# Kernel optimization log

Hardware: AMD Instinct MI355X
Metric: run time of the kernel (lower is better)

## Reference

```python
import jax, jax.numpy as jnp
import numpy as np

T, B = 64, 32
POS_V, WORD_V = 48, 32000
P_EMB, W_EMB = 128, 512
P_HID, W_HID = 256, 1024


def setup_inputs() -> dict:
    key = jax.random.key(0)
    ks = iter(jax.random.split(key, 40))
    def prm(shape, s=0.05):
        return jax.random.normal(next(ks), shape, dtype=jnp.float32) * s
    z = lambda *shape: jnp.zeros(shape, jnp.float32)
    inp = {
        'pos': jax.random.randint(next(ks), (T, B), 0, POS_V),
        'word': jax.random.randint(next(ks), (T, B), 0, WORD_V),
        'pos_emb_W': prm((POS_V, P_EMB)),
        'word_emb_W': prm((WORD_V, W_EMB)),
        'w2p_W': prm((W_HID, W_HID)), 'w2p_b': z(W_HID),
        'p2w_W': prm((P_HID, P_HID)), 'p2w_b': z(P_HID),
        'p_Wih0': prm((4 * P_HID, P_EMB + W_HID)), 'p_Whh0': prm((4 * P_HID, P_HID)),
        'p_bih0': z(4 * P_HID), 'p_bhh0': z(4 * P_HID),
        'w_Wih0': prm((4 * W_HID, W_EMB + P_HID)), 'w_Whh0': prm((4 * W_HID, W_HID)),
        'w_bih0': z(4 * W_HID), 'w_bhh0': z(4 * W_HID),
        'w_Wih1': prm((4 * W_HID, W_HID)), 'w_Whh1': prm((4 * W_HID, W_HID)),
        'w_bih1': z(4 * W_HID), 'w_bhh1': z(4 * W_HID),
        'pos_proj_W': prm((POS_V, P_HID)), 'pos_proj_b': z(POS_V),
        'word_proj1_W': prm((W_EMB, W_HID)), 'word_proj1_b': z(W_EMB),
        'word_proj2_b': z(WORD_V),
    }
    return inp


def _lstm_cell(x, h, c, Wih, Whh, bih, bhh):
    # PyTorch LSTMCell: gates ordered i, f, g, o
    g = x @ Wih.T + h @ Whh.T + bih + bhh
    i, f, gg, o = jnp.split(g, 4, axis=-1)
    c_new = jax.nn.sigmoid(f) * c + jax.nn.sigmoid(i) * jnp.tanh(gg)
    h_new = jax.nn.sigmoid(o) * jnp.tanh(c_new)
    return h_new, c_new


def reference(pos, word, pos_emb_W, word_emb_W, w2p_W, w2p_b, p2w_W, p2w_b,
              p_Wih0, p_Whh0, p_bih0, p_bhh0,
              w_Wih0, w_Whh0, w_bih0, w_bhh0,
              w_Wih1, w_Whh1, w_bih1, w_bhh1,
              pos_proj_W, pos_proj_b, word_proj1_W, word_proj1_b, word_proj2_b):
    p_emb = pos_emb_W[pos]    # [T, B, P_EMB]
    w_emb = word_emb_W[word]  # [T, B, W_EMB]
    Bn = pos.shape[1]
    p_layers = [(p_Wih0, p_Whh0, p_bih0, p_bhh0)]
    w_layers = [(w_Wih0, w_Whh0, w_bih0, w_bhh0), (w_Wih1, w_Whh1, w_bih1, w_bhh1)]
    ph = p_Whh0.shape[1]
    wh = w_Whh0.shape[1]
    init = (jnp.zeros((1, Bn, ph), jnp.float32), jnp.zeros((1, Bn, ph), jnp.float32),
            jnp.zeros((2, Bn, wh), jnp.float32), jnp.zeros((2, Bn, wh), jnp.float32))

    def step(carry, xs):
        p_h, p_c, w_h, w_c = carry
        p_t, w_t = xs
        # word_gate on word-RNN last hidden at t-1, conditions POS-RNN at t
        last_w = jnp.tanh(w_h[-1] @ w2p_W.T + w2p_b)
        x = jnp.concatenate([p_t, last_w], axis=-1)
        new_ph, new_pc = [], []
        for li, (Wih, Whh, bih, bhh) in enumerate(p_layers):
            h, c = _lstm_cell(x, p_h[li], p_c[li], Wih, Whh, bih, bhh)
            new_ph.append(h); new_pc.append(c); x = h
        p_out = jax.nn.log_softmax(x @ pos_proj_W.T + pos_proj_b, axis=-1)
        # pos_gate on POS-RNN last hidden at t, conditions word-RNN at t
        last_p = jnp.tanh(new_ph[-1] @ p2w_W.T + p2w_b)
        x = jnp.concatenate([w_t, last_p], axis=-1)
        new_wh, new_wc = [], []
        for li, (Wih, Whh, bih, bhh) in enumerate(w_layers):
            h, c = _lstm_cell(x, w_h[li], w_c[li], Wih, Whh, bih, bhh)
            new_wh.append(h); new_wc.append(c); x = h
        # tied word projection: hid -> emb -> vocab with embedding weight
        w_logits = (x @ word_proj1_W.T + word_proj1_b) @ word_emb_W.T + word_proj2_b
        w_out = jax.nn.log_softmax(w_logits, axis=-1)
        carry = (jnp.stack(new_ph), jnp.stack(new_pc), jnp.stack(new_wh), jnp.stack(new_wc))
        return carry, (p_out, w_out)

    _, (p_outs, w_outs) = jax.lax.scan(step, init, (p_emb, w_emb))
    return p_outs, w_outs
```

## Files before the change

kernel.cpp:

```cpp
#include <hip/hip_runtime.h>
#include <math.h>

#define LSTR 36

__device__ __forceinline__ void gbar(unsigned* cnts, int idx, unsigned nb)
{
    __syncthreads();
    if (threadIdx.x == 0) {
        __threadfence();
        __hip_atomic_fetch_add(&cnts[idx], 1u, __ATOMIC_ACQ_REL,
                               __HIP_MEMORY_SCOPE_AGENT);
        while (__hip_atomic_load(&cnts[idx], __ATOMIC_RELAXED,
                                 __HIP_MEMORY_SCOPE_AGENT) < nb)
            __builtin_amdgcn_s_sleep(2);
        __threadfence();
    }
    __syncthreads();
}

__device__ __forceinline__ void gemm_core(
    const float* __restrict__ A, int lda,
    const float* __restrict__ W, int ldw,
    int n0, int N, int K,
    const float* __restrict__ b1, const float* __restrict__ b2,
    int act, float* __restrict__ C, int ldc, int row0,
    float* As, float* Ws)
{
    const int tid = threadIdx.x;
    const int jl = tid & 15;
    const int bg = tid >> 4;
    float acc[4][4] = {{0.f,0.f,0.f,0.f},{0.f,0.f,0.f,0.f},{0.f,0.f,0.f,0.f},{0.f,0.f,0.f,0.f}};

    float4 ra[2], rw[4];
    int ar[2], akv[2], wr[4], wkv[4];
#pragma unroll
    for (int p = 0; p < 2; ++p) {
        int i = tid + 128 * p;
        ar[p] = i >> 3; akv[p] = (i & 7) << 2;
    }
#pragma unroll
    for (int p = 0; p < 4; ++p) {
        int i = tid + 128 * p;
        wr[p] = i >> 3; wkv[p] = (i & 7) << 2;
    }

#pragma unroll
    for (int p = 0; p < 2; ++p)
        ra[p] = *(const float4*)(A + (size_t)(row0 + ar[p]) * lda + akv[p]);
#pragma unroll
    for (int p = 0; p < 4; ++p) {
        int n = n0 + wr[p];
        rw[p] = (n < N) ? *(const float4*)(W + (size_t)n * ldw + wkv[p])
                        : make_float4(0.f, 0.f, 0.f, 0.f);
    }

    for (int kk = 0; kk < K; kk += 32) {
#pragma unroll
        for (int p = 0; p < 2; ++p)
            *(float4*)&As[ar[p] * LSTR + akv[p]] = ra[p];
#pragma unroll
        for (int p = 0; p < 4; ++p)
            *(float4*)&Ws[wr[p] * LSTR + wkv[p]] = rw[p];
        __syncthreads();

        if (kk + 32 < K) {
            int kn = kk + 32;
#pragma unroll
            for (int p = 0; p < 2; ++p)
                ra[p] = *(const float4*)(A + (size_t)(row0 + ar[p]) * lda + kn + akv[p]);
#pragma unroll
            for (int p = 0; p < 4; ++p) {
                int n = n0 + wr[p];
                rw[p] = (n < N) ? *(const float4*)(W + (size_t)n * ldw + kn + wkv[p])
                                : make_float4(0.f, 0.f, 0.f, 0.f);
            }
        }

#pragma unroll
        for (int k4 = 0; k4 < 8; ++k4) {
            float4 av[4], wv[4];
#pragma unroll
            for (int jb = 0; jb < 4; ++jb) av[jb] = *(float4*)&As[(bg + 8 * jb) * LSTR + k4 * 4];
#pragma unroll
            for (int jn = 0; jn < 4; ++jn) wv[jn] = *(float4*)&Ws[(jl + 16 * jn) * LSTR + k4 * 4];
#pragma unroll
            for (int jn = 0; jn < 4; ++jn)
#pragma unroll
                for (int jb = 0; jb < 4; ++jb) {
                    acc[jn][jb] += av[jb].x * wv[jn].x;
                    acc[jn][jb] += av[jb].y * wv[jn].y;
                    acc[jn][jb] += av[jb].z * wv[jn].z;
                    acc[jn][jb] += av[jb].w * wv[jn].w;
                }
        }
        __syncthreads();
    }

#pragma unroll
    for (int jn = 0; jn < 4; ++jn) {
        int n = n0 + jl + 16 * jn;
        if (n < N) {
            float bb = (b1 ? b1[n] : 0.f) + (b2 ? b2[n] : 0.f);
#pragma unroll
            for (int jb = 0; jb < 4; ++jb) {
                int b = bg + 8 * jb;
                float x = acc[jn][jb] + bb;
                if (act == 1) x = tanhf(x);
                C[(size_t)(row0 + b) * ldc + n] = x;
            }
        }
    }
}

__global__ void __launch_bounds__(128) gemm_generic(
    const float* __restrict__ A, int lda, const float* __restrict__ W, int ldw,
    const float* __restrict__ b1, const float* __restrict__ b2,
    float* __restrict__ C, int ldc, int N, int K, int act, int swapxy)
{
    __shared__ __align__(16) float As[32 * LSTR];
    __shared__ __align__(16) float Ws[64 * LSTR];
    int bn = swapxy ? blockIdx.y : blockIdx.x;
    int bm = swapxy ? blockIdx.x : blockIdx.y;
    gemm_core(A, lda, W, ldw, bn * 64, N, K, b1, b2, act, C, ldc, bm * 32, As, Ws);
}

__device__ __forceinline__ void lstm_core(
    const float* __restrict__ A, int K,
    const float* __restrict__ Wih, int ldw, int H,
    const float* __restrict__ addA, int ldA,
    const float* __restrict__ addB, int ldB,
    float* __restrict__ h_out, float* __restrict__ c_state,
    int blk, float* As, float* Ws)
{
    const int tid = threadIdx.x;
    const int jl = tid & 15;
    const int bg = tid >> 4;
    const int j0 = blk * 16;
    float acc[4][4] = {{0.f,0.f,0.f,0.f},{0.f,0.f,0.f,0.f},{0.f,0.f,0.f,0.f},{0.f,0.f,0.f,0.f}};

    float4 ra[2], rw[4];
    int ar[2], akv[2], wr[4], wkv[4], wrow[4];
#pragma unroll
    for (int p = 0; p < 2; ++p) {
        int i = tid + 128 * p;
        ar[p] = i >> 3; akv[p] = (i & 7) << 2;
    }
#pragma unroll
    for (int p = 0; p < 4; ++p) {
        int i = tid + 128 * p;
        wr[p] = i >> 3; wkv[p] = (i & 7) << 2;
        wrow[p] = (wr[p] >> 4) * H + j0 + (wr[p] & 15);
    }

#pragma unroll
    for (int p = 0; p < 2; ++p)
        ra[p] = *(const float4*)(A + (size_t)ar[p] * K + akv[p]);
#pragma unroll
    for (int p = 0; p < 4; ++p)
        rw[p] = *(const float4*)(Wih + (size_t)wrow[p] * ldw + wkv[p]);

    for (int kk = 0; kk < K; kk += 32) {
#pragma unroll
        for (int p = 0; p < 2; ++p)
            *(float4*)&As[ar[p] * LSTR + akv[p]] = ra[p];
#pragma unroll
        for (int p = 0; p < 4; ++p)
            *(float4*)&Ws[wr[p] * LSTR + wkv[p]] = rw[p];
        __syncthreads();

        if (kk + 32 < K) {
            int kn = kk + 32;
#pragma unroll
            for (int p = 0; p < 2; ++p)
                ra[p] = *(const float4*)(A + (size_t)ar[p] * K + kn + akv[p]);
#pragma unroll
            for (int p = 0; p < 4; ++p)
                rw[p] = *(const float4*)(Wih + (size_t)wrow[p] * ldw + kn + wkv[p]);
        }

#pragma unroll
        for (int k4 = 0; k4 < 8; ++k4) {
            float4 av[4], wv[4];
#pragma unroll
            for (int jb = 0; jb < 4; ++jb) av[jb] = *(float4*)&As[(bg + 8 * jb) * LSTR + k4 * 4];
#pragma unroll
            for (int jn = 0; jn < 4; ++jn) wv[jn] = *(float4*)&Ws[(jl + 16 * jn) * LSTR + k4 * 4];
#pragma unroll
            for (int jn = 0; jn < 4; ++jn)
#pragma unroll
                for (int jb = 0; jb < 4; ++jb) {
                    acc[jn][jb] += av[jb].x * wv[jn].x;
                    acc[jn][jb] += av[jb].y * wv[jn].y;
                    acc[jn][jb] += av[jb].z * wv[jn].z;
                    acc[jn][jb] += av[jb].w * wv[jn].w;
                }
        }
        __syncthreads();
    }

    const int j = j0 + jl;
#pragma unroll
    for (int jb = 0; jb < 4; ++jb) {
        int b = bg + 8 * jb;
        float g[4];
#pragma unroll
        for (int jn = 0; jn < 4; ++jn) {
            int row = jn * H + j;
            float x = acc[jn][jb];
            if (addA) x += addA[(size_t)b * ldA + row];
            if (addB) x += addB[(size_t)b * ldB + row];
            g[jn] = x;
        }
        float c_old = c_state[b * H + j];
        float ii = 1.f / (1.f + expf(-g[0]));
        float ff = 1.f / (1.f + expf(-g[1]));
        float gg = tanhf(g[2]);
        float oo = 1.f / (1.f + expf(-g[3]));
        float cn = ff * c_old + ii * gg;
        float hn = oo * tanhf(cn);
        c_state[b * H + j] = cn;
        h_out[b * H + j] = hn;
    }
}

struct RecArgs {
    const float *w2p_W, *w2p_b, *p_Whh0;
    const float *w_Whh0, *w_Whh1, *w_bih1, *w_bhh1;
    const float *p_Wih0, *p2w_W, *p2w_b, *w_Wih0, *w_Wih1;
    const float *Ap, *Aw;
    float *u, *hp_hh, *w0_hh, *w1_hh, *v;
    float *Hp, *Hw1, *h_w0, *c_p, *c_w0, *c_w1;
    unsigned *bar;
};

__global__ void __launch_bounds__(128) recurrence(RecArgs a)
{
    __shared__ __align__(16) float As[32 * LSTR];
    __shared__ __align__(16) float Ws[64 * LSTR];
    const int blk = blockIdx.x;
    const unsigned nb = gridDim.x;
    int bi = 0;

    for (int t = 0; t < 64; ++t) {
        const float* hw1 = a.Hw1 + (size_t)t * 32 * 1024;
        const float* hp  = a.Hp  + (size_t)t * 32 * 256;

        if (blk < 16)
            gemm_core(hw1, 1024, a.w2p_W, 1024, blk * 64, 1024, 1024,
                      a.w2p_b, nullptr, 1, a.u, 1024, 0, As, Ws);
        else if (blk < 32)
            gemm_core(hp, 256, a.p_Whh0, 256, (blk - 16) * 64, 1024, 256,
                      nullptr, nullptr, 0, a.hp_hh, 1024, 0, As, Ws);
        else if (blk < 96)
            gemm_core(a.h_w0, 1024, a.w_Whh0, 1024, (blk - 32) * 64, 4096, 1024,
                      nullptr, nullptr, 0, a.w0_hh, 4096, 0, As, Ws);
        else
            gemm_core(hw1, 1024, a.w_Whh1, 1024, (blk - 96) * 64, 4096, 1024,
                      a.w_bih1, a.w_bhh1, 0, a.w1_hh, 4096, 0, As, Ws);
        gbar(a.bar, bi++, nb);

        if (blk < 16)
            lstm_core(a.u, 1024, a.p_Wih0 + 128, 1152, 256,
                      a.Ap + (size_t)t * 32 * 1024, 1024, a.hp_hh, 1024,
                      a.Hp + (size_t)(t + 1) * 32 * 256, a.c_p, blk, As, Ws);
        gbar(a.bar, bi++, nb);

        if (blk < 4)
            gemm_core(a.Hp + (size_t)(t + 1) * 32 * 256, 256, a.p2w_W, 256,
                      blk * 64, 256, 256, a.p2w_b, nullptr, 1, a.v, 256, 0, As, Ws);
        gbar(a.bar, bi++, nb);

        if (blk < 64)
            lstm_core(a.v, 256, a.w_Wih0 + 512, 768, 1024,
                      a.Aw + (size_t)t * 32 * 4096, 4096, a.w0_hh, 4096,
                      a.h_w0, a.c_w0, blk, As, Ws);
        gbar(a.bar, bi++, nb);

        if (blk < 64)
            lstm_core(a.h_w0, 1024, a.w_Wih1, 1024, 1024,
                      nullptr, 0, a.w1_hh, 4096,
                      a.Hw1 + (size_t)(t + 1) * 32 * 1024, a.c_w1, blk, As, Ws);
        gbar(a.bar, bi++, nb);
    }
}

__global__ void __launch_bounds__(128) gather_emb(
    const int* __restrict__ pos, const int* __restrict__ word,
    const float* __restrict__ pe, const float* __restrict__ we,
    float* __restrict__ Xp, float* __restrict__ Xw)
{
    int row = blockIdx.x;
    int p = pos[row];
    int w = word[row];
    for (int i = threadIdx.x; i < 128; i += 128)
        Xp[(size_t)row * 128 + i] = pe[(size_t)p * 128 + i];
    for (int i = threadIdx.x; i < 512; i += 128)
        Xw[(size_t)row * 512 + i] = we[(size_t)w * 512 + i];
}

__global__ void __launch_bounds__(256) pos_out_k(
    const float* __restrict__ Hp, const float* __restrict__ W,
    const float* __restrict__ bias, float* __restrict__ out)
{
    int row = blockIdx.x * 4 + (threadIdx.x >> 6);
    int lane = threadIdx.x & 63;
    const float* h = Hp + (size_t)row * 256;
    float logit = -INFINITY;
    if (lane < 48) {
        float s = bias[lane];
        const float* w = W + (size_t)lane * 256;
        for (int k = 0; k < 256; k += 4) {
            s += h[k] * w[k];
            s += h[k + 1] * w[k + 1];
            s += h[k + 2] * w[k + 2];
            s += h[k + 3] * w[k + 3];
        }
        logit = s;
    }
    float m = logit;
    for (int off = 1; off < 64; off <<= 1) m = fmaxf(m, __shfl_xor(m, off));
    float e = (lane < 48) ? expf(logit - m) : 0.f;
    float ssum = e;
    for (int off = 1; off < 64; off <<= 1) ssum += __shfl_xor(ssum, off);
    float ls = m + logf(ssum);
    if (lane < 48) out[(size_t)row * 48 + lane] = logit - ls;
}

__global__ void __launch_bounds__(256) logsoftmax_w(float* __restrict__ out)
{
    __shared__ float redm[256], reds[256];
    int row = blockIdx.x;
    float* p = out + (size_t)row * 32000;
    float4* p4 = (float4*)p;
    int tid = threadIdx.x;

    float m = -INFINITY, s = 0.f;
    for (int i = tid; i < 8000; i += 256) {
        float4 v = p4[i];
        float x;
        x = v.x; if (x > m) { s = s * expf(m - x) + 1.f; m = x; } else s += expf(x - m);
        x = v.y; if (x > m) { s = s * expf(m - x) + 1.f; m = x; } else s += expf(x - m);
        x = v.z; if (x > m) { s = s * expf(m - x) + 1.f; m = x; } else s += expf(x - m);
        x = v.w; if (x > m) { s = s * expf(m - x) + 1.f; m = x; } else s += expf(x - m);
    }
    redm[tid] = m; reds[tid] = s;
    __syncthreads();
    for (int st = 128; st > 0; st >>= 1) {
        if (tid < st) {
            float m2 = redm[tid + st], s2 = reds[tid + st];
            float M = fmaxf(redm[tid], m2);
            reds[tid] = reds[tid] * expf(redm[tid] - M) + s2 * expf(m2 - M);
            redm[tid] = M;
        }
        __syncthreads();
    }
    float ls = redm[0] + logf(reds[0]);

    for (int i = tid; i < 8000; i += 256) {
        float4 v = p4[i];
        v.x -= ls; v.y -= ls; v.z -= ls; v.w -= ls;
        p4[i] = v;
    }
}

extern "C" void kernel_launch(void* const* d_in, const int* in_sizes, int n_in,
                              void* d_out, int out_size, void* d_ws, size_t ws_size,
                              hipStream_t stream)
{
    const int T = 64, B = 32, TB = T * B;

    const int*   pos         = (const int*)d_in[0];
    const int*   word        = (const int*)d_in[1];
    const float* pos_emb_W   = (const float*)d_in[2];
    const float* word_emb_W  = (const float*)d_in[3];
    const float* w2p_W       = (const float*)d_in[4];
    const float* w2p_b       = (const float*)d_in[5];
    const float* p2w_W       = (const float*)d_in[6];
    const float* p2w_b       = (const float*)d_in[7];
    const float* p_Wih0      = (const float*)d_in[8];
    const float* p_Whh0      = (const float*)d_in[9];
    const float* p_bih0      = (const float*)d_in[10];
    const float* p_bhh0      = (const float*)d_in[11];
    const float* w_Wih0      = (const float*)d_in[12];
    const float* w_Whh0      = (const float*)d_in[13];
    const float* w_bih0      = (const float*)d_in[14];
    const float* w_bhh0      = (const float*)d_in[15];
    const float* w_Wih1      = (const float*)d_in[16];
    const float* w_Whh1      = (const float*)d_in[17];
    const float* w_bih1      = (const float*)d_in[18];
    const float* w_bhh1      = (const float*)d_in[19];
    const float* pos_proj_W  = (const float*)d_in[20];
    const float* pos_proj_b  = (const float*)d_in[21];
    const float* word_proj1W = (const float*)d_in[22];
    const float* word_proj1b = (const float*)d_in[23];
    const float* word_proj2b = (const float*)d_in[24];

    float* out   = (float*)d_out;
    float* Pout  = out;
    float* Wout  = out + (size_t)TB * 48;

    float* ws = (float*)d_ws;
    size_t off = 0;
    auto alloc = [&](size_t n) { float* p = ws + off; off += n; return p; };
    float* Xp    = alloc((size_t)TB * 128);
    float* Xw    = alloc((size_t)TB * 512);
    float* Ap    = alloc((size_t)TB * 1024);
    float* Hp    = alloc((size_t)(TB + B) * 256);
    float* Hw1   = alloc((size_t)(TB + B) * 1024);
    float* E     = alloc((size_t)TB * 512);
    float* c_p   = alloc((size_t)B * 256);
    float* h_w0  = alloc((size_t)B * 1024);
    float* c_w0  = alloc((size_t)B * 1024);
    float* c_w1  = alloc((size_t)B * 1024);
    float* u     = alloc((size_t)B * 1024);
    float* v     = alloc((size_t)B * 256);
    float* hp_hh = alloc((size_t)B * 1024);
    float* w0_hh = alloc((size_t)B * 4096);
    float* w1_hh = alloc((size_t)B * 4096);
    unsigned* bar = (unsigned*)alloc(512);

    float* Aw = Wout;

    hipMemsetAsync(c_p, 0, (size_t)(B * 256 + 3 * B * 1024) * 4, stream);
    hipMemsetAsync(Hp,  0, (size_t)B * 256 * 4, stream);
    hipMemsetAsync(Hw1, 0, (size_t)B * 1024 * 4, stream);
    hipMemsetAsync(bar, 0, 512 * 4, stream);

    gather_emb<<<TB, 128, 0, stream>>>(pos, word, pos_emb_W, word_emb_W, Xp, Xw);
    gemm_generic<<<dim3(16, 64), 128, 0, stream>>>(Xp, 128, p_Wih0, 1152,
        p_bih0, p_bhh0, Ap, 1024, 1024, 128, 0, 0);
    gemm_generic<<<dim3(64, 64), 128, 0, stream>>>(Xw, 512, w_Wih0, 768,
        w_bih0, w_bhh0, Aw, 4096, 4096, 512, 0, 0);

    RecArgs ra;
    ra.w2p_W = w2p_W; ra.w2p_b = w2p_b; ra.p_Whh0 = p_Whh0;
    ra.w_Whh0 = w_Whh0; ra.w_Whh1 = w_Whh1; ra.w_bih1 = w_bih1; ra.w_bhh1 = w_bhh1;
    ra.p_Wih0 = p_Wih0; ra.p2w_W = p2w_W; ra.p2w_b = p2w_b;
    ra.w_Wih0 = w_Wih0; ra.w_Wih1 = w_Wih1;
    ra.Ap = Ap; ra.Aw = Aw;
    ra.u = u; ra.hp_hh = hp_hh; ra.w0_hh = w0_hh; ra.w1_hh = w1_hh; ra.v = v;
    ra.Hp = Hp; ra.Hw1 = Hw1; ra.h_w0 = h_w0;
    ra.c_p = c_p; ra.c_w0 = c_w0; ra.c_w1 = c_w1;
    ra.bar = bar;
    recurrence<<<160, 128, 0, stream>>>(ra);

    gemm_generic<<<dim3(8, 64), 128, 0, stream>>>(Hw1 + 32 * 1024, 1024,
        word_proj1W, 1024, word_proj1b, nullptr, E, 512, 512, 1024, 0, 0);
    gemm_generic<<<dim3(64, 500), 128, 0, stream>>>(E, 512, word_emb_W, 512,
        word_proj2b, nullptr, Wout, 32000, 32000, 512, 0, 1);
    logsoftmax_w<<<TB, 256, 0, stream>>>(Wout);
    pos_out_k<<<TB / 4, 256, 0, stream>>>(Hp + 32 * 256, pos_proj_W, pos_proj_b, Pout);
}
```

Measured before the change: 30.00 ms.

## Make recurrence weights register-resident with per-stage flag dataflow instead of grid barriers

Measured after the change: 36.17 ms. +20.6%, slower.

```diff
diff --git a/kernel.cpp b/kernel.cpp
--- a/kernel.cpp
+++ b/kernel.cpp
@@ -2,21 +2,6 @@
 #include <math.h>
 
 #define LSTR 36
-
-__device__ __forceinline__ void gbar(unsigned* cnts, int idx, unsigned nb)
-{
-    __syncthreads();
-    if (threadIdx.x == 0) {
-        __threadfence();
-        __hip_atomic_fetch_add(&cnts[idx], 1u, __ATOMIC_ACQ_REL,
-                               __HIP_MEMORY_SCOPE_AGENT);
-        while (__hip_atomic_load(&cnts[idx], __ATOMIC_RELAXED,
-                                 __HIP_MEMORY_SCOPE_AGENT) < nb)
-            __builtin_amdgcn_s_sleep(2);
-        __threadfence();
-    }
-    __syncthreads();
-}
 
 __device__ __forceinline__ void gemm_core(
     const float* __restrict__ A, int lda,
@@ -124,163 +109,301 @@
     gemm_core(A, lda, W, ldw, bn * 64, N, K, b1, b2, act, C, ldc, bm * 32, As, Ws);
 }
 
-__device__ __forceinline__ void lstm_core(
-    const float* __restrict__ A, int K,
-    const float* __restrict__ Wih, int ldw, int H,
+
+#define FU   0
+#define FPHP 1
+#define FB   2
+#define FV   3
+#define FW0  4
+#define FD   5
+#define FW1  6
+#define FE   7
+
+__device__ __forceinline__ void flag_set(unsigned* F, int idx)
+{
+    __syncthreads();
+    if (threadIdx.x == 0) {
+        __threadfence();
+        __hip_atomic_fetch_add(&F[idx], 1u, __ATOMIC_RELEASE,
+                               __HIP_MEMORY_SCOPE_AGENT);
+    }
+}
+
+__device__ __forceinline__ void flag_wait(unsigned* F, int idx, unsigned need)
+{
+    if (threadIdx.x == 0) {
+        while (__hip_atomic_load(&F[idx], __ATOMIC_RELAXED,
+                                 __HIP_MEMORY_SCOPE_AGENT) < need)
+            __builtin_amdgcn_s_sleep(2);
+        __threadfence();
+    }
+    __syncthreads();
+}
+
+template<int KS>
+__device__ __forceinline__ void rr_load_w(
+    float4 (&Wv)[4][16], const float* __restrict__ W, int ldw, int kofs,
+    int r0, int r1, int r2, int r3)
+{
+    const int l  = threadIdx.x & 63;
+    const int ks = l % KS;
+    const int k0 = kofs + ks * 64;
+    const float* p0 = W + (size_t)r0 * ldw + k0;
+    const float* p1 = W + (size_t)r1 * ldw + k0;
+    const float* p2 = W + (size_t)r2 * ldw + k0;
+    const float* p3 = W + (size_t)r3 * ldw + k0;
+#pragma unroll
+    for (int f4 = 0; f4 < 16; ++f4) {
+        Wv[0][f4] = *(const float4*)(p0 + f4 * 4);
+        Wv[1][f4] = *(const float4*)(p1 + f4 * 4);
+        Wv[2][f4] = *(const float4*)(p2 + f4 * 4);
+        Wv[3][f4] = *(const float4*)(p3 + f4 * 4);
+    }
+}
+
+template<int KS, int MODE>
+__device__ __forceinline__ void rr_core(
+    float4 (&Wv)[4][16],
+    const float* __restrict__ hsrc,
+    float* __restrict__ hl,
+    int c0, int c1,
+    float* __restrict__ Cout, int ldc, int nbase, float4 bias, int act,
+    int j, int H,
     const float* __restrict__ addA, int ldA,
     const float* __restrict__ addB, int ldB,
-    float* __restrict__ h_out, float* __restrict__ c_state,
-    int blk, float* As, float* Ws)
+    float* __restrict__ h_out, float* __restrict__ c_st)
 {
     const int tid = threadIdx.x;
-    const int jl = tid & 15;
-    const int bg = tid >> 4;
-    const int j0 = blk * 16;
-    float acc[4][4] = {{0.f,0.f,0.f,0.f},{0.f,0.f,0.f,0.f},{0.f,0.f,0.f,0.f},{0.f,0.f,0.f,0.f}};
-
-    float4 ra[2], rw[4];
-    int ar[2], akv[2], wr[4], wkv[4], wrow[4];
-#pragma unroll
-    for (int p = 0; p < 2; ++p) {
-        int i = tid + 128 * p;
-        ar[p] = i >> 3; akv[p] = (i & 7) << 2;
-    }
-#pragma unroll
-    for (int p = 0; p < 4; ++p) {
-        int i = tid + 128 * p;
-        wr[p] = i >> 3; wkv[p] = (i & 7) << 2;
-        wrow[p] = (wr[p] >> 4) * H + j0 + (wr[p] & 15);
-    }
-
-#pragma unroll
-    for (int p = 0; p < 2; ++p)
-        ra[p] = *(const float4*)(A + (size_t)ar[p] * K + akv[p]);
-#pragma unroll
-    for (int p = 0; p < 4; ++p)
-        rw[p] = *(const float4*)(Wih + (size_t)wrow[p] * ldw + wkv[p]);
-
-    for (int kk = 0; kk < K; kk += 32) {
-#pragma unroll
-        for (int p = 0; p < 2; ++p)
-            *(float4*)&As[ar[p] * LSTR + akv[p]] = ra[p];
-#pragma unroll
-        for (int p = 0; p < 4; ++p)
-            *(float4*)&Ws[wr[p] * LSTR + wkv[p]] = rw[p];
+    const int l   = tid & 63;
+    const int ks  = l % KS;
+    const int K   = KS * 64;
+    const int F4B = K / 4;
+    const int NF4 = K / 128;
+
+    float4 st[NF4];
+#pragma unroll
+    for (int p = 0; p < NF4; ++p) {
+        int i  = tid + 256 * p;
+        int bl = i / F4B;
+        int kk = (i % F4B) * 4;
+        st[p] = *(const float4*)(hsrc + (size_t)(c0 * 8 + bl) * K + kk);
+    }
+
+    for (int c = c0; c < c1; ++c) {
+#pragma unroll
+        for (int p = 0; p < NF4; ++p) {
+            int i  = tid + 256 * p;
+            int bl = i / F4B;
+            int kk = (i % F4B) * 4;
+            *(float4*)&hl[(bl * KS + (kk >> 6)) * 68 + (kk & 63)] = st[p];
+        }
         __syncthreads();
-
-        if (kk + 32 < K) {
-            int kn = kk + 32;
-#pragma unroll
-            for (int p = 0; p < 2; ++p)
-                ra[p] = *(const float4*)(A + (size_t)ar[p] * K + kn + akv[p]);
-#pragma unroll
-            for (int p = 0; p < 4; ++p)
-                rw[p] = *(const float4*)(Wih + (size_t)wrow[p] * ldw + kn + wkv[p]);
-        }
-
-#pragma unroll
-        for (int k4 = 0; k4 < 8; ++k4) {
-            float4 av[4], wv[4];
-#pragma unroll
-            for (int jb = 0; jb < 4; ++jb) av[jb] = *(float4*)&As[(bg + 8 * jb) * LSTR + k4 * 4];
-#pragma unroll
-            for (int jn = 0; jn < 4; ++jn) wv[jn] = *(float4*)&Ws[(jl + 16 * jn) * LSTR + k4 * 4];
-#pragma unroll
-            for (int jn = 0; jn < 4; ++jn)
-#pragma unroll
-                for (int jb = 0; jb < 4; ++jb) {
-                    acc[jn][jb] += av[jb].x * wv[jn].x;
-                    acc[jn][jb] += av[jb].y * wv[jn].y;
-                    acc[jn][jb] += av[jb].z * wv[jn].z;
-                    acc[jn][jb] += av[jb].w * wv[jn].w;
+        if (c + 1 < c1) {
+#pragma unroll
+            for (int p = 0; p < NF4; ++p) {
+                int i  = tid + 256 * p;
+                int bl = i / F4B;
+                int kk = (i % F4B) * 4;
+                st[p] = *(const float4*)(hsrc + (size_t)((c + 1) * 8 + bl) * K + kk);
+            }
+        }
+
+        float acc[4][8];
+#pragma unroll
+        for (int m = 0; m < 4; ++m)
+#pragma unroll
+            for (int bl = 0; bl < 8; ++bl) acc[m][bl] = 0.f;
+
+#pragma unroll
+        for (int bl = 0; bl < 8; ++bl)
+#pragma unroll
+            for (int f4 = 0; f4 < 16; ++f4) {
+                float4 hv = *(float4*)&hl[(bl * KS + ks) * 68 + f4 * 4];
+#pragma unroll
+                for (int m = 0; m < 4; ++m) {
+                    acc[m][bl] += Wv[m][f4].x * hv.x;
+                    acc[m][bl] += Wv[m][f4].y * hv.y;
+                    acc[m][bl] += Wv[m][f4].z * hv.z;
+                    acc[m][bl] += Wv[m][f4].w * hv.w;
                 }
-        }
+            }
         __syncthreads();
-    }
-
-    const int j = j0 + jl;
-#pragma unroll
-    for (int jb = 0; jb < 4; ++jb) {
-        int b = bg + 8 * jb;
-        float g[4];
-#pragma unroll
-        for (int jn = 0; jn < 4; ++jn) {
-            int row = jn * H + j;
-            float x = acc[jn][jb];
-            if (addA) x += addA[(size_t)b * ldA + row];
-            if (addB) x += addB[(size_t)b * ldB + row];
-            g[jn] = x;
-        }
-        float c_old = c_state[b * H + j];
-        float ii = 1.f / (1.f + expf(-g[0]));
-        float ff = 1.f / (1.f + expf(-g[1]));
-        float gg = tanhf(g[2]);
-        float oo = 1.f / (1.f + expf(-g[3]));
-        float cn = ff * c_old + ii * gg;
-        float hn = oo * tanhf(cn);
-        c_state[b * H + j] = cn;
-        h_out[b * H + j] = hn;
+
+#pragma unroll
+        for (int off = KS / 2; off >= 1; off >>= 1)
+#pragma unroll
+            for (int m = 0; m < 4; ++m)
+#pragma unroll
+                for (int bl = 0; bl < 8; ++bl)
+                    acc[m][bl] += __shfl_xor(acc[m][bl], off);
+
+#pragma unroll
+        for (int bl = 0; bl < 8; ++bl) {
+            if ((bl % KS) == ks) {
+                int b = c * 8 + bl;
+                if (MODE == 0) {
+                    float r0 = acc[0][bl] + bias.x;
+                    float r1 = acc[1][bl] + bias.y;
+                    float r2 = acc[2][bl] + bias.z;
+                    float r3 = acc[3][bl] + bias.w;
+                    if (act) { r0 = tanhf(r0); r1 = tanhf(r1); r2 = tanhf(r2); r3 = tanhf(r3); }
+                    float4 o = make_float4(r0, r1, r2, r3);
+                    *(float4*)&Cout[(size_t)b * ldc + nbase] = o;
+                } else {
+                    float g[4];
+#pragma unroll
+                    for (int m = 0; m < 4; ++m) {
+                        float x = acc[m][bl];
+                        if (addA) x += addA[(size_t)b * ldA + m * H + j];
+                        if (addB) x += addB[(size_t)b * ldB + m * H + j];
+                        g[m] = x;
+                    }
+                    float co = c_st[(size_t)b * H + j];
+                    float ii = 1.f / (1.f + expf(-g[0]));
+                    float ff = 1.f / (1.f + expf(-g[1]));
+                    float gg = tanhf(g[2]);
+                    float oo = 1.f / (1.f + expf(-g[3]));
+                    float cn = ff * co + ii * gg;
+                    float hn = oo * tanhf(cn);
+                    c_st[(size_t)b * H + j] = cn;
+                    h_out[(size_t)b * H + j] = hn;
+                }
+            }
+        }
     }
 }
 
 struct RecArgs {
-    const float *w2p_W, *w2p_b, *p_Whh0;
+    const float *w2p_W, *w2p_b, *p_Whh0, *p2w_W, *p2w_b;
+    const float *p_Wih0, *w_Wih0, *w_Wih1;
     const float *w_Whh0, *w_Whh1, *w_bih1, *w_bhh1;
-    const float *p_Wih0, *p2w_W, *p2w_b, *w_Wih0, *w_Wih1;
     const float *Ap, *Aw;
-    float *u, *hp_hh, *w0_hh, *w1_hh, *v;
+    float *u, *v, *hp_hh, *w0_hh, *w1_hh;
     float *Hp, *Hw1, *h_w0, *c_p, *c_w0, *c_w1;
-    unsigned *bar;
+    unsigned *flags;
 };
 
-__global__ void __launch_bounds__(128) recurrence(RecArgs a)
-{
-    __shared__ __align__(16) float As[32 * LSTR];
-    __shared__ __align__(16) float Ws[64 * LSTR];
+__global__ void __launch_bounds__(256, 1) recurrence_rr(RecArgs a)
+{
+    __shared__ __align__(16) float hl[8 * 16 * 68];
     const int blk = blockIdx.x;
-    const unsigned nb = gridDim.x;
-    int bi = 0;
-
-    for (int t = 0; t < 64; ++t) {
-        const float* hw1 = a.Hw1 + (size_t)t * 32 * 1024;
-        const float* hp  = a.Hp  + (size_t)t * 32 * 256;
-
-        if (blk < 16)
-            gemm_core(hw1, 1024, a.w2p_W, 1024, blk * 64, 1024, 1024,
-                      a.w2p_b, nullptr, 1, a.u, 1024, 0, As, Ws);
-        else if (blk < 32)
-            gemm_core(hp, 256, a.p_Whh0, 256, (blk - 16) * 64, 1024, 256,
-                      nullptr, nullptr, 0, a.hp_hh, 1024, 0, As, Ws);
-        else if (blk < 96)
-            gemm_core(a.h_w0, 1024, a.w_Whh0, 1024, (blk - 32) * 64, 4096, 1024,
-                      nullptr, nullptr, 0, a.w0_hh, 4096, 0, As, Ws);
-        else
-            gemm_core(hw1, 1024, a.w_Whh1, 1024, (blk - 96) * 64, 4096, 1024,
-                      a.w_bih1, a.w_bhh1, 0, a.w1_hh, 4096, 0, As, Ws);
-        gbar(a.bar, bi++, nb);
-
-        if (blk < 16)
-            lstm_core(a.u, 1024, a.p_Wih0 + 128, 1152, 256,
-                      a.Ap + (size_t)t * 32 * 1024, 1024, a.hp_hh, 1024,
-                      a.Hp + (size_t)(t + 1) * 32 * 256, a.c_p, blk, As, Ws);
-        gbar(a.bar, bi++, nb);
-
-        if (blk < 4)
-            gemm_core(a.Hp + (size_t)(t + 1) * 32 * 256, 256, a.p2w_W, 256,
-                      blk * 64, 256, 256, a.p2w_b, nullptr, 1, a.v, 256, 0, As, Ws);
-        gbar(a.bar, bi++, nb);
-
-        if (blk < 64)
-            lstm_core(a.v, 256, a.w_Wih0 + 512, 768, 1024,
-                      a.Aw + (size_t)t * 32 * 4096, 4096, a.w0_hh, 4096,
-                      a.h_w0, a.c_w0, blk, As, Ws);
-        gbar(a.bar, bi++, nb);
-
-        if (blk < 64)
-            lstm_core(a.h_w0, 1024, a.w_Wih1, 1024, 1024,
-                      nullptr, 0, a.w1_hh, 4096,
-                      a.Hw1 + (size_t)(t + 1) * 32 * 1024, a.c_w1, blk, As, Ws);
-        gbar(a.bar, bi++, nb);
+    const int tid = threadIdx.x;
+    const int l = tid & 63, w = tid >> 6;
+    unsigned* F = a.flags;
+
+    if (blk < 64) {
+        const int rg = l / 16;
+        const int nb = blk * 64 + w * 16 + rg * 4;
+        float4 Wv[4][16];
+        rr_load_w<16>(Wv, a.w_Whh1, 1024, 0, nb, nb + 1, nb + 2, nb + 3);
+        float4 bias = make_float4(
+            a.w_bih1[nb] + a.w_bhh1[nb], a.w_bih1[nb+1] + a.w_bhh1[nb+1],
+            a.w_bih1[nb+2] + a.w_bhh1[nb+2], a.w_bih1[nb+3] + a.w_bhh1[nb+3]);
+        for (int t = 0; t < 64; ++t) {
+            if (t) flag_wait(F, (t-1)*8 + FE, 64);
+            rr_core<16,0>(Wv, a.Hw1 + (size_t)t*32*1024, hl, 0, 4,
+                          a.w1_hh, 4096, nb, bias, 0,
+                          0, 0, nullptr, 0, nullptr, 0, nullptr, nullptr);
+            flag_set(F, t*8 + FW1);
+        }
+    } else if (blk < 128) {
+        const int rg = l / 16;
+        const int nb = (blk - 64) * 64 + w * 16 + rg * 4;
+        float4 Wv[4][16];
+        rr_load_w<16>(Wv, a.w_Whh0, 1024, 0, nb, nb + 1, nb + 2, nb + 3);
+        float4 bias = make_float4(0.f, 0.f, 0.f, 0.f);
+        for (int t = 0; t < 64; ++t) {
+            if (t) flag_wait(F, (t-1)*8 + FD, 16);
+            rr_core<16,0>(Wv, a.h_w0, hl, 0, 4,
+                          a.w0_hh, 4096, nb, bias, 0,
+                          0, 0, nullptr, 0, nullptr, 0, nullptr, nullptr);
+            flag_set(F, t*8 + FW0);
+        }
+    } else if (blk < 144) {
+        const int rg = l / 16;
+        const int nb = (blk - 128) * 64 + w * 16 + rg * 4;
+        float4 Wv[4][16];
+        rr_load_w<16>(Wv, a.w2p_W, 1024, 0, nb, nb + 1, nb + 2, nb + 3);
+        float4 bias = make_float4(a.w2p_b[nb], a.w2p_b[nb+1], a.w2p_b[nb+2], a.w2p_b[nb+3]);
+        for (int t = 0; t < 64; ++t) {
+            if (t) flag_wait(F, (t-1)*8 + FE, 64);
+            rr_core<16,0>(Wv, a.Hw1 + (size_t)t*32*1024, hl, 0, 4,
+                          a.u, 1024, nb, bias, 1,
+                          0, 0, nullptr, 0, nullptr, 0, nullptr, nullptr);
+            flag_set(F, t*8 + FU);
+        }
+    } else if (blk < 148) {
+        const int rg = l / 4;
+        const int nb = (blk - 144) * 256 + w * 64 + rg * 4;
+        float4 Wv[4][16];
+        rr_load_w<4>(Wv, a.p_Whh0, 256, 0, nb, nb + 1, nb + 2, nb + 3);
+        float4 bias = make_float4(0.f, 0.f, 0.f, 0.f);
+        for (int t = 0; t < 64; ++t) {
+            if (t) flag_wait(F, (t-1)*8 + FB, 16);
+            rr_core<4,0>(Wv, a.Hp + (size_t)t*32*256, hl, 0, 4,
+                         a.hp_hh, 1024, nb, bias, 0,
+                         0, 0, nullptr, 0, nullptr, 0, nullptr, nullptr);
+            flag_set(F, t*8 + FPHP);
+        }
+    } else if (blk < 164) {
+        const int rg = l / 16;
+        const int j = (blk - 148) * 16 + w * 4 + rg;
+        float4 Wv[4][16];
+        rr_load_w<16>(Wv, a.p_Wih0, 1152, 128, j, 256 + j, 512 + j, 768 + j);
+        float4 bias = make_float4(0.f, 0.f, 0.f, 0.f);
+        for (int t = 0; t < 64; ++t) {
+            flag_wait(F, t*8 + FU, 16);
+            flag_wait(F, t*8 + FPHP, 4);
+            rr_core<16,1>(Wv, a.u, hl, 0, 4,
+                          nullptr, 0, 0, bias, 0,
+                          j, 256, a.Ap + (size_t)t*32*1024, 1024, a.hp_hh, 1024,
+                          a.Hp + (size_t)(t+1)*32*256, a.c_p);
+            flag_set(F, t*8 + FB);
+        }
+    } else if (blk < 168) {
+        const int rg = l / 4;
+        const int nb = w * 64 + rg * 4;
+        const int c0 = blk - 164;
+        float4 Wv[4][16];
+        rr_load_w<4>(Wv, a.p2w_W, 256, 0, nb, nb + 1, nb + 2, nb + 3);
+        float4 bias = make_float4(a.p2w_b[nb], a.p2w_b[nb+1], a.p2w_b[nb+2], a.p2w_b[nb+3]);
+        for (int t = 0; t < 64; ++t) {
+            flag_wait(F, t*8 + FB, 16);
+            rr_core<4,0>(Wv, a.Hp + (size_t)(t+1)*32*256, hl, c0, c0 + 1,
+                         a.v, 256, nb, bias, 1,
+                         0, 0, nullptr, 0, nullptr, 0, nullptr, nullptr);
+            flag_set(F, t*8 + FV);
+        }
+    } else if (blk < 184) {
+        const int rg = l / 4;
+        const int j = (blk - 168) * 64 + w * 16 + rg;
+        float4 Wv[4][16];
+        rr_load_w<4>(Wv, a.w_Wih0, 768, 512, j, 1024 + j, 2048 + j, 3072 + j);
+        float4 bias = make_float4(0.f, 0.f, 0.f, 0.f);
+        for (int t = 0; t < 64; ++t) {
+            flag_wait(F, t*8 + FV, 4);
+            flag_wait(F, t*8 + FW0, 64);
+            rr_core<4,1>(Wv, a.v, hl, 0, 4,
+                         nullptr, 0, 0, bias, 0,
+                         j, 1024, a.Aw + (size_t)t*32*4096, 4096, a.w0_hh, 4096,
+                         a.h_w0, a.c_w0);
+            flag_set(F, t*8 + FD);
+        }
+    } else {
+        const int rg = l / 16;
+        const int j = (blk - 184) * 16 + w * 4 + rg;
+        float4 Wv[4][16];
+        rr_load_w<16>(Wv, a.w_Wih1, 1024, 0, j, 1024 + j, 2048 + j, 3072 + j);
+        float4 bias = make_float4(0.f, 0.f, 0.f, 0.f);
+        for (int t = 0; t < 64; ++t) {
+            flag_wait(F, t*8 + FD, 16);
+            flag_wait(F, t*8 + FW1, 64);
+            rr_core<16,1>(Wv, a.h_w0, hl, 0, 4,
+                          nullptr, 0, 0, bias, 0,
+                          j, 1024, nullptr, 0, a.w1_hh, 4096,
+                          a.Hw1 + (size_t)(t+1)*32*1024, a.c_w1);
+            flag_set(F, t*8 + FE);
+        }
     }
 }
 
@@ -417,14 +540,14 @@
     float* hp_hh = alloc((size_t)B * 1024);
     float* w0_hh = alloc((size_t)B * 4096);
     float* w1_hh = alloc((size_t)B * 4096);
-    unsigned* bar = (unsigned*)alloc(512);
+    unsigned* flags = (unsigned*)alloc(512);
 
     float* Aw = Wout;
 
     hipMemsetAsync(c_p, 0, (size_t)(B * 256 + 3 * B * 1024) * 4, stream);
     hipMemsetAsync(Hp,  0, (size_t)B * 256 * 4, stream);
     hipMemsetAsync(Hw1, 0, (size_t)B * 1024 * 4, stream);
-    hipMemsetAsync(bar, 0, 512 * 4, stream);
+    hipMemsetAsync(flags, 0, 512 * 4, stream);
 
     gather_emb<<<TB, 128, 0, stream>>>(pos, word, pos_emb_W, word_emb_W, Xp, Xw);
     gemm_generic<<<dim3(16, 64), 128, 0, stream>>>(Xp, 128, p_Wih0, 1152,
@@ -434,15 +557,15 @@
 
     RecArgs ra;
     ra.w2p_W = w2p_W; ra.w2p_b = w2p_b; ra.p_Whh0 = p_Whh0;
+    ra.p2w_W = p2w_W; ra.p2w_b = p2w_b;
+    ra.p_Wih0 = p_Wih0; ra.w_Wih0 = w_Wih0; ra.w_Wih1 = w_Wih1;
     ra.w_Whh0 = w_Whh0; ra.w_Whh1 = w_Whh1; ra.w_bih1 = w_bih1; ra.w_bhh1 = w_bhh1;
-    ra.p_Wih0 = p_Wih0; ra.p2w_W = p2w_W; ra.p2w_b = p2w_b;
-    ra.w_Wih0 = w_Wih0; ra.w_Wih1 = w_Wih1;
     ra.Ap = Ap; ra.Aw = Aw;
-    ra.u = u; ra.hp_hh = hp_hh; ra.w0_hh = w0_hh; ra.w1_hh = w1_hh; ra.v = v;
+    ra.u = u; ra.v = v; ra.hp_hh = hp_hh; ra.w0_hh = w0_hh; ra.w1_hh = w1_hh;
     ra.Hp = Hp; ra.Hw1 = Hw1; ra.h_w0 = h_w0;
     ra.c_p = c_p; ra.c_w0 = c_w0; ra.c_w1 = c_w1;
-    ra.bar = bar;
-    recurrence<<<160, 128, 0, stream>>>(ra);
+    ra.flags = flags;
+    recurrence_rr<<<248, 256, 0, stream>>>(ra);
 
     gemm_generic<<<dim3(8, 64), 128, 0, stream>>>(Hw1 + 32 * 1024, 1024,
         word_proj1W, 1024, word_proj1b, nullptr, E, 512, 512, 1024, 0, 0);
```
